# Kernel tuning notes

Hardware: AMD Instinct MI355X
Metric: run time of the kernel (lower is better)

## Reference

```python
import jax, jax.numpy as jnp
import numpy as np

B, N, D, F, OUT = 2048, 784, 10, 2, 10
EPS = 1e-12


def setup_inputs() -> dict:
    key = jax.random.key(0)
    k1, k2, k3, k4 = jax.random.split(key, 4)
    x = jax.random.uniform(k1, (B, N), dtype=jnp.float32)  # pixel values in [0,1]
    # xavier-uniform-like init matching the torch module's std formulas
    std0 = (2.0 / (F + F * D)) ** 0.5
    core0 = jax.random.uniform(k2, (1, F, D), jnp.float32, -std0, std0)
    stdm = (2.0 / (D * F + F * D)) ** 0.5
    cores_mid = jax.random.uniform(k3, (N - 1, D, F, D), jnp.float32, -stdm, stdm)
    classifier = jax.random.normal(k4, (OUT, D), jnp.float32) * 0.1
    return {"x": x, "core0": core0, "cores_mid": cores_mid, "classifier": classifier}


def reference(x, core0, cores_mid, classifier):
    Bsz = x.shape[0]
    xf = x.reshape(Bsz, -1)                      # [B, N]
    feats = jnp.stack([1.0 - xf, xf], axis=-1)   # [B, N, F] feature map

    # per-site contraction of cores with features (all sites at once)
    head = jnp.einsum('ldh,bd->blh', core0, feats[:, 0])            # [B, 1, D]
    tail = jnp.einsum('nldh,bnd->bnlh', cores_mid, feats[:, 1:])    # [B, N-1, D, D]

    log_norm = jnp.zeros(Bsz, dtype=x.dtype)
    # log-depth binary tree contraction; shapes shrink by ~half each level
    # (static shapes per level -> Python while is jit-compatible)
    while tail.shape[1] > 0:
        # pair 0: head (left-boundary tensor) with next tensor
        nh = head @ tail[:, 0]                                      # [B, 1, D]
        hn = jnp.maximum(jnp.sqrt(jnp.sum(nh * nh, axis=(-2, -1))), EPS)
        log_norm = log_norm + jnp.log(hn)
        head = nh / hn[:, None, None]
        # remaining tensors paired (t1,t2),(t3,t4),... ; odd leftover is carried
        rest = tail[:, 1:]
        p = rest.shape[1] // 2
        a = rest[:, 0:2 * p:2]                                      # [B, p, D, D]
        b = rest[:, 1:2 * p:2]                                      # [B, p, D, D]
        c = a @ b                                                   # [B, p, D, D]
        norms = jnp.maximum(jnp.sqrt(jnp.sum(c * c, axis=(-2, -1))), EPS)  # [B, p]
        log_norm = log_norm + jnp.sum(jnp.log(norms), axis=1)
        c = c / norms[..., None, None]
        tail = jnp.concatenate([c, rest[:, 2 * p:]], axis=1)
    mps_output = head[:, 0]                                         # [B, D]
    logits = mps_output @ classifier.T + log_norm[:, None]          # [B, OUT]
    return logits
```

## Files before the change

### kernel.cpp

```cpp
#include <hip/hip_runtime.h>


constexpr int Bsz = 2048;
constexpr int Nn  = 784;
constexpr int NS  = 783;
constexpr int LCH = 16;
constexpr int NCH = (NS + LCH - 1) / LCH;

#define PKH_FMA(d, a, b, c) \
  asm("v_pk_fma_f16 %0, %1, %2, %3" : "=v"(d) : "v"(a), "v"(b), "v"(c))
#define PKH_ACC_LO(d, m, s) \
  asm("v_pk_fma_f16 %0, %1, %2, %0 op_sel:[0,0,0] op_sel_hi:[1,0,1]" \
      : "+v"(d) : "v"(m), "v"(s))
#define PKH_ACC_HI(d, m, s) \
  asm("v_pk_fma_f16 %0, %1, %2, %0 op_sel:[0,1,0] op_sel_hi:[1,1,1]" \
      : "+v"(d) : "v"(m), "v"(s))
#define PKH_MUL_LO(d, m, s) \
  asm("v_pk_mul_f16 %0, %1, %2 op_sel:[0,0] op_sel_hi:[1,0]" \
      : "=v"(d) : "v"(m), "v"(s))
#define CVT_H2F(f, u) asm("v_cvt_f32_f16 %0, %1" : "=v"(f) : "v"(u))

__device__ __forceinline__ unsigned short f2h_bits(float f) {
    union { _Float16 h; unsigned short u; } c;
    c.h = (_Float16)f;
    return c.u;
}
__device__ __forceinline__ float hlo(unsigned u) {
    union { unsigned short s; _Float16 h; } c;
    c.s = (unsigned short)(u & 0xffff);
    return (float)c.h;
}
__device__ __forceinline__ float hhi(unsigned u) {
    union { unsigned short s; _Float16 h; } c;
    c.s = (unsigned short)(u >> 16);
    return (float)c.h;
}

__device__ __forceinline__ void site_step(const unsigned* __restrict__ ws,
                                          const unsigned x2,
                                          const unsigned (&src)[5][5],
                                          unsigned (&dst)[5][5]) {
#pragma unroll
    for (int ip = 0; ip < 5; ++ip) {
        unsigned m[10];
        const uint4* w4 = (const uint4*)(ws + ip * 20);
#pragma unroll
        for (int t = 0; t < 5; ++t) {
            const uint4 w = w4[t];
            PKH_FMA(m[2 * t],     w.y, x2, w.x);
            PKH_FMA(m[2 * t + 1], w.w, x2, w.z);
        }
#pragma unroll
        for (int r = 0; r < 5; ++r) {
            if (ip == 0) {
#pragma unroll
                for (int q = 0; q < 5; ++q) PKH_MUL_LO(dst[r][q], m[q], src[r][0]);
            } else {
#pragma unroll
                for (int q = 0; q < 5; ++q) PKH_ACC_LO(dst[r][q], m[q], src[r][ip]);
            }
#pragma unroll
            for (int q = 0; q < 5; ++q) PKH_ACC_HI(dst[r][q], m[5 + q], src[r][ip]);
        }
    }
}

__global__ __launch_bounds__(256, 3) void chunk_kernel(
    const float* __restrict__ x, const float* __restrict__ cores,
    unsigned* __restrict__ pbuf, float* __restrict__ lbuf) {
    __shared__ unsigned s_w[LCH * 100];
    __shared__ float    s_x[128 * 17];

    const int c   = blockIdx.y;
    const int n0  = 1 + c * LCH;
    const int n1  = min(n0 + LCH, Nn);
    const int ns  = n1 - n0;
    const int tid = (int)threadIdx.x;
    const int b0  = (int)blockIdx.x * 128;

    for (int e = tid; e < ns * 50; e += 256) {
        const int k = e / 50, s = e - k * 50;
        const int i = s / 5, q = s - i * 5;
        const float* g = cores + (size_t)(n0 - 1 + k) * 200 + i * 20 + 2 * q;
        const float a0 = g[0], a1 = g[1], bb0 = g[10], bb1 = g[11];
        const unsigned A = ((unsigned)f2h_bits(2.f * a1) << 16) | f2h_bits(2.f * a0);
        const unsigned D = ((unsigned)f2h_bits(2.f * (bb1 - a1)) << 16) |
                           f2h_bits(2.f * (bb0 - a0));
        s_w[k * 100 + 2 * s]     = A;
        s_w[k * 100 + 2 * s + 1] = D;
    }
    for (int e = tid; e < 128 * 16; e += 256) {
        const int bl = e >> 4, k = e & 15;
        if (k < ns) s_x[bl * 17 + k] = x[(size_t)(b0 + bl) * Nn + n0 + k];
    }
    __syncthreads();

    const int h = tid & 1;
    const int u = tid >> 1;
    const int b = b0 + u;
    const float* __restrict__ xs = s_x + u * 17;

    unsigned p[5][5], q2[5][5];
    {
        const unsigned short xb = f2h_bits(xs[0]);
        const unsigned x2 = ((unsigned)xb << 16) | xb;
#pragma unroll
        for (int r = 0; r < 5; ++r)
#pragma unroll
            for (int q = 0; q < 5; ++q) {
                const unsigned A = s_w[(5 * h + r) * 10 + 2 * q];
                const unsigned D = s_w[(5 * h + r) * 10 + 2 * q + 1];
                PKH_FMA(p[r][q], D, x2, A);
            }
    }
    int k = 1;
    while (k + 1 < ns) {
        {
            const unsigned short xb = f2h_bits(xs[k]);
            site_step(s_w + k * 100, ((unsigned)xb << 16) | xb, p, q2);
        }
        {
            const unsigned short xb = f2h_bits(xs[k + 1]);
            site_step(s_w + (k + 1) * 100, ((unsigned)xb << 16) | xb, q2, p);
        }
        k += 2;
    }
    if (k < ns) {
        const unsigned short xb = f2h_bits(xs[k]);
        site_step(s_w + k * 100, ((unsigned)xb << 16) | xb, p, q2);
#pragma unroll
        for (int r = 0; r < 5; ++r)
#pragma unroll
            for (int q = 0; q < 5; ++q) p[r][q] = q2[r][q];
    }

    float ss = 0.f;
#pragma unroll
    for (int r = 0; r < 5; ++r)
#pragma unroll
        for (int q = 0; q < 5; ++q) {
            const float lo = hlo(p[r][q]), hi = hhi(p[r][q]);
            ss = fmaf(lo, lo, ss);
            ss = fmaf(hi, hi, ss);
        }
    ss += __shfl_xor(ss, 1);
    ss = fmaxf(ss, 1e-30f);
    const float rin = rsqrtf(ss);
    if (h == 0)
        lbuf[(size_t)c * Bsz + b] = 0.5f * __logf(ss) - (float)ns * 0.69314718056f;

    unsigned* dst = pbuf + ((size_t)c * Bsz + b) * 50;
#pragma unroll
    for (int r = 0; r < 5; ++r)
#pragma unroll
        for (int q = 0; q < 5; ++q) {
            const float lo = hlo(p[r][q]) * rin;
            const float hi = hhi(p[r][q]) * rin;
            dst[(5 * h + r) * 5 + q] =
                ((unsigned)f2h_bits(hi) << 16) | f2h_bits(lo);
        }
}

__global__ __launch_bounds__(64, 1) void combine_kernel(
    const float* __restrict__ x, const float* __restrict__ core0,
    const float* __restrict__ cls, const unsigned* __restrict__ pbuf,
    const float* __restrict__ lbuf, float* __restrict__ out, int C) {
    __shared__ __align__(16) unsigned ring[8][256];

    const int tid   = (int)threadIdx.x;
    const int j     = tid & 15;
    const int jj    = (j < 10) ? j : 9;
    const int gbase = tid & 48;
    const int sl    = tid >> 4;
    const int b     = (int)blockIdx.x * 4 + sl;
    const int qoff  = jj >> 1;
    const unsigned sh = (unsigned)(jj & 1) * 16;

    float v[10];
    const float x0 = x[(size_t)b * Nn];
#pragma unroll
    for (int i = 0; i < 10; ++i) {
        const float c0 = core0[i], c1 = core0[10 + i];
        v[i] = fmaf(x0, c1 - c0, c0);
    }
    float llog = 0.f;
    for (int cc = j; cc < C; cc += 16)
        llog += lbuf[(size_t)cc * Bsz + b];
    llog += __shfl_xor(llog, 1);
    llog += __shfl_xor(llog, 2);
    llog += __shfl_xor(llog, 4);
    llog += __shfl_xor(llog, 8);

    const int flat = (tid * 4 <= 196) ? tid * 4 : 196;
    const unsigned* gsrc0 = pbuf + (size_t)blockIdx.x * 200 + flat;
    const size_t cstride = (size_t)Bsz * 50;

#define STAGE(cc)                                                          \
    __builtin_amdgcn_global_load_lds(                                      \
        (const __attribute__((address_space(1))) unsigned*)(gsrc0 +        \
            (size_t)(cc) * cstride),                                       \
        (__attribute__((address_space(3))) unsigned*)&ring[(cc) & 7][0],   \
        16, 0, 0)

#pragma unroll
    for (int d = 0; d < 7; ++d) STAGE(d);

    const int lbase = sl * 50 + qoff;
    for (int c = 0; c < C; ++c) {
        const int d = c & 7;
        if (c + 7 <= C - 1) {
            asm volatile("s_waitcnt vmcnt(6)" ::: "memory");
        } else {
            asm volatile("s_waitcnt vmcnt(0)" ::: "memory");
        }
        __builtin_amdgcn_sched_barrier(0);

        float acc = 0.f;
#pragma unroll
        for (int i = 0; i < 10; ++i) {
            unsigned ud = ring[d][lbase + i * 5] >> sh;
            float wv;
            CVT_H2F(wv, ud);
            acc = fmaf(v[i], wv, acc);
        }
        if (j >= 10) acc = 0.f;
        if ((c & 7) == 7 || c == C - 1) {
            float s = acc * acc;
            s += __shfl_xor(s, 1);
            s += __shfl_xor(s, 2);
            s += __shfl_xor(s, 4);
            s += __shfl_xor(s, 8);
            s = fmaxf(s, 1e-30f);
            llog += 0.5f * __logf(s);
            acc *= rsqrtf(s);
        }
#pragma unroll
        for (int i = 0; i < 10; ++i) v[i] = __shfl(acc, gbase + i);

        if (c + 7 < C) STAGE(c + 7);
    }
#undef STAGE

    if (j < 10) {
        float acc = llog;
#pragma unroll
        for (int i = 0; i < 10; ++i) acc = fmaf(v[i], cls[j * 10 + i], acc);
        out[(size_t)b * 10 + j] = acc;
    }
}

extern "C" void kernel_launch(void* const* d_in, const int* in_sizes, int n_in,
                              void* d_out, int out_size, void* d_ws, size_t ws_size,
                              hipStream_t stream) {
    const float* x     = (const float*)d_in[0];
    const float* core0 = (const float*)d_in[1];
    const float* cores = (const float*)d_in[2];
    const float* cls   = (const float*)d_in[3];
    float* out = (float*)d_out;

    const int C = NCH;
    unsigned* pbuf = (unsigned*)d_ws;
    float*    lbuf = (float*)(pbuf + (size_t)C * Bsz * 50);

    hipLaunchKernelGGL(chunk_kernel, dim3(Bsz / 128, C), dim3(256),
                       0, stream, x, cores, pbuf, lbuf);
    hipLaunchKernelGGL(combine_kernel, dim3(Bsz / 4), dim3(64),
                       0, stream, x, core0, cls, pbuf, lbuf, out, C);
}
```

Baseline: 72.19 us.

## Compute full site matrix first and update state row-wise in place

The ping-pong state buffers are replaced by a single 5x5 packed-half state. All 50 site-matrix entries are materialized first, then each state row is accumulated into a 5-register temporary and written back in place. This frees the second 25-register state array, and launch bounds are raised from 3 to 4 blocks per CU to use the saved registers for occupancy. In exchange, the 50-entry matrix stays live for the whole row update, and the 2x-unrolled loop becomes a simple per-site loop, which may reduce instruction-level overlap.

```diff
diff --git a/kernel.cpp b/kernel.cpp
--- a/kernel.cpp
+++ b/kernel.cpp
@@ -36,36 +36,7 @@
     return (float)c.h;
 }
 
-__device__ __forceinline__ void site_step(const unsigned* __restrict__ ws,
-                                          const unsigned x2,
-                                          const unsigned (&src)[5][5],
-                                          unsigned (&dst)[5][5]) {
-#pragma unroll
-    for (int ip = 0; ip < 5; ++ip) {
-        unsigned m[10];
-        const uint4* w4 = (const uint4*)(ws + ip * 20);
-#pragma unroll
-        for (int t = 0; t < 5; ++t) {
-            const uint4 w = w4[t];
-            PKH_FMA(m[2 * t],     w.y, x2, w.x);
-            PKH_FMA(m[2 * t + 1], w.w, x2, w.z);
-        }
-#pragma unroll
-        for (int r = 0; r < 5; ++r) {
-            if (ip == 0) {
-#pragma unroll
-                for (int q = 0; q < 5; ++q) PKH_MUL_LO(dst[r][q], m[q], src[r][0]);
-            } else {
-#pragma unroll
-                for (int q = 0; q < 5; ++q) PKH_ACC_LO(dst[r][q], m[q], src[r][ip]);
-            }
-#pragma unroll
-            for (int q = 0; q < 5; ++q) PKH_ACC_HI(dst[r][q], m[5 + q], src[r][ip]);
-        }
-    }
-}
-
-__global__ __launch_bounds__(256, 3) void chunk_kernel(
+__global__ __launch_bounds__(256, 4) void chunk_kernel(
     const float* __restrict__ x, const float* __restrict__ cores,
     unsigned* __restrict__ pbuf, float* __restrict__ lbuf) {
     __shared__ unsigned s_w[LCH * 100];
@@ -100,7 +71,7 @@
     const int b = b0 + u;
     const float* __restrict__ xs = s_x + u * 17;
 
-    unsigned p[5][5], q2[5][5];
+    unsigned p[5][5];
     {
         const unsigned short xb = f2h_bits(xs[0]);
         const unsigned x2 = ((unsigned)xb << 16) | xb;
@@ -113,25 +84,45 @@
                 PKH_FMA(p[r][q], D, x2, A);
             }
     }
-    int k = 1;
-    while (k + 1 < ns) {
-        {
-            const unsigned short xb = f2h_bits(xs[k]);
-            site_step(s_w + k * 100, ((unsigned)xb << 16) | xb, p, q2);
-        }
-        {
-            const unsigned short xb = f2h_bits(xs[k + 1]);
-            site_step(s_w + (k + 1) * 100, ((unsigned)xb << 16) | xb, q2, p);
-        }
-        k += 2;
-    }
-    if (k < ns) {
+
+    for (int k = 1; k < ns; ++k) {
         const unsigned short xb = f2h_bits(xs[k]);
-        site_step(s_w + k * 100, ((unsigned)xb << 16) | xb, p, q2);
-#pragma unroll
-        for (int r = 0; r < 5; ++r)
-#pragma unroll
-            for (int q = 0; q < 5; ++q) p[r][q] = q2[r][q];
+        const unsigned x2 = ((unsigned)xb << 16) | xb;
+        const unsigned* ws = s_w + k * 100;
+
+        unsigned Mf[50];
+#pragma unroll
+        for (int ip = 0; ip < 5; ++ip) {
+            const uint4* w4 = (const uint4*)(ws + ip * 20);
+#pragma unroll
+            for (int t = 0; t < 5; ++t) {
+                const uint4 w = w4[t];
+                PKH_FMA(Mf[ip * 10 + 2 * t],     w.y, x2, w.x);
+                PKH_FMA(Mf[ip * 10 + 2 * t + 1], w.w, x2, w.z);
+            }
+        }
+
+#pragma unroll
+        for (int r = 0; r < 5; ++r) {
+            unsigned acc[5];
+#pragma unroll
+            for (int q = 0; q < 5; ++q)
+                PKH_MUL_LO(acc[q], Mf[q], p[r][0]);
+#pragma unroll
+            for (int q = 0; q < 5; ++q)
+                PKH_ACC_HI(acc[q], Mf[5 + q], p[r][0]);
+#pragma unroll
+            for (int ip = 1; ip < 5; ++ip) {
+#pragma unroll
+                for (int q = 0; q < 5; ++q)
+                    PKH_ACC_LO(acc[q], Mf[ip * 10 + q], p[r][ip]);
+#pragma unroll
+                for (int q = 0; q < 5; ++q)
+                    PKH_ACC_HI(acc[q], Mf[ip * 10 + 5 + q], p[r][ip]);
+            }
+#pragma unroll
+            for (int q = 0; q < 5; ++q) p[r][q] = acc[q];
+        }
     }
 
     float ss = 0.f;
```

New measurement: 72.58 us. Within noise of the previous version (+0.6%).
